# Kernel optimization log

Hardware: AMD Instinct MI355X
Metric: run time of the kernel (lower is better)

The kernel has to match this reference:

```python
import jax, jax.numpy as jnp
import numpy as np

# Base model: 2-layer ReLU MLP, D->H->O, state flattened as [w1, b1, w2, b2]
D, H, O = 32, 64, 1
T = 1024          # xtype_size (number of tickers)
M = 8             # mesa_parameter_size
N = 32768         # rows
S = H * D + H + O * H + O  # 2177, flattened state size


def setup_inputs() -> dict:
    key = jax.random.key(0)
    ks = jax.random.split(key, 6)
    x = jax.random.normal(ks[0], (N, D), dtype=jnp.float32)
    ticker = jax.random.randint(ks[1], (N,), 0, T, dtype=jnp.int32)
    mesa_layer_weight = jax.random.uniform(ks[2], (M, T), jnp.float32, -0.1, 0.1)
    meta_layer_weight = jax.random.uniform(ks[3], (S, M), jnp.float32, -0.1, 0.1)
    meta_layer_bias = jnp.zeros((S,), jnp.float32)
    base_state = jax.random.normal(ks[4], (S,), dtype=jnp.float32) * 0.05
    return {"x": x, "ticker": ticker,
            "mesa_layer_weight": mesa_layer_weight,
            "meta_layer_weight": meta_layer_weight,
            "meta_layer_bias": meta_layer_bias,
            "base_state": base_state}


def _unflatten(states):
    # states: [T, S] -> per-ticker MLP params
    i0 = H * D
    i1 = i0 + H
    i2 = i1 + O * H
    w1 = states[:, :i0].reshape(T, H, D)
    b1 = states[:, i0:i1]                  # [T, H]
    w2 = states[:, i1:i2].reshape(T, O, H)
    b2 = states[:, i2:]                    # [T, O]
    return w1, b1, w2, b2


def reference(x, ticker, mesa_layer_weight, meta_layer_weight, meta_layer_bias, base_state):
    # F.linear(one_hot_i, mesa_W) selects column i -> all mesa states = mesa_W.T : [T, M]
    # temp = meta_W @ mesa_state for every ticker at once: [T, S]
    temps = jnp.einsum('mt,sm->ts', mesa_layer_weight, meta_layer_weight)
    # allow_meta mask is all-ones (allow_meta_structure=None); dropout p=0 is identity
    states = base_state[None, :] + meta_layer_bias[None, :] + temps  # [T, S]
    w1, b1, w2, b2 = _unflatten(states)
    # gather per-row ticker params and run the base MLP forward
    h = jax.nn.relu(jnp.einsum('nd,nhd->nh', x, w1[ticker]) + b1[ticker])  # [N, H]
    out = jnp.einsum('nh,noh->no', h, w2[ticker]) + b2[ticker]             # [N, O]
    return out
```

## Files before the change

kernel.cpp:

```cpp
#include <hip/hip_runtime.h>


#define DD 32
#define TT 1024
#define MM 8
#define KB 8

__global__ __launch_bounds__(1024, 4) void fused_kernel(
    const float* __restrict__ x,
    const int*   __restrict__ ticker,
    const float* __restrict__ mesa,
    const float* __restrict__ metaw,
    const float* __restrict__ metab,
    const float* __restrict__ base,
    float* __restrict__ out)
{
    __shared__ float4 U4[32 * 2 * 64];
    __shared__ float4 B1q[8 * 64];
    __shared__ float4 Ub1[2 * 64];
    __shared__ float4 U2q[2 * 64];
    __shared__ float  B1b[64];
    __shared__ float  B2b[64];

    const int tid  = threadIdx.x;
    const int lane = tid & 63;
    const int dm   = tid >> 6;

    #pragma unroll
    for (int i2 = 0; i2 < 4; ++i2) {
        int idx = dm * 4 + i2;
        int d = idx >> 1, m4 = idx & 1;
        U4[(d * 2 + m4) * 64 + lane] =
            *(const float4*)(metaw + ((lane * 32 + d) * MM + m4 * 4));
    }
    if (dm < 8) {
        int s0 = lane * 32 + dm * 4;
        float4 bv = *(const float4*)(base  + s0);
        float4 mv = *(const float4*)(metab + s0);
        B1q[dm * 64 + lane] = make_float4(bv.x + mv.x, bv.y + mv.y, bv.z + mv.z, bv.w + mv.w);
    } else if (dm < 10) {
        int m4 = dm - 8;
        Ub1[m4 * 64 + lane] = *(const float4*)(metaw + ((2048 + lane) * MM + m4 * 4));
    } else if (dm < 12) {
        int m4 = dm - 10;
        U2q[m4 * 64 + lane] = *(const float4*)(metaw + ((2112 + lane) * MM + m4 * 4));
    } else if (dm == 12) {
        B1b[lane] = base[2048 + lane] + metab[2048 + lane];
    } else if (dm == 13) {
        B2b[lane] = base[2112 + lane] + metab[2112 + lane];
    }
    __syncthreads();

    const int n0 = blockIdx.x * 128 + dm * KB;

    float xr[4];
    #pragma unroll
    for (int r = 0; r < 4; ++r) xr[r] = x[n0 * DD + r * 64 + lane];

    float4 g0[KB], g1[KB];
    float  c0[KB];
    #pragma unroll
    for (int i = 0; i < KB; ++i) {
        g0[i] = make_float4(0.f, 0.f, 0.f, 0.f);
        g1[i] = make_float4(0.f, 0.f, 0.f, 0.f);
        c0[i] = 0.f;
    }

    for (int dq = 0; dq < 8; ++dq) {
        float4 bq = B1q[dq * 64 + lane];
        #pragma unroll
        for (int dd = 0; dd < 4; ++dd) {
            int d = dq * 4 + dd;
            float4 u0 = U4[(d * 2 + 0) * 64 + lane];
            float4 u1 = U4[(d * 2 + 1) * 64 + lane];
            float bs = (dd == 0) ? bq.x : (dd == 1) ? bq.y : (dd == 2) ? bq.z : bq.w;
            #pragma unroll
            for (int i = 0; i < KB; ++i) {
                int lidx = (i & 1) * 32 + d;
                float xv = __uint_as_float(
                    __builtin_amdgcn_readlane(__float_as_uint(xr[i >> 1]), lidx));
                c0[i]   = fmaf(xv, bs,   c0[i]);
                g0[i].x = fmaf(xv, u0.x, g0[i].x);
                g0[i].y = fmaf(xv, u0.y, g0[i].y);
                g0[i].z = fmaf(xv, u0.z, g0[i].z);
                g0[i].w = fmaf(xv, u0.w, g0[i].w);
                g1[i].x = fmaf(xv, u1.x, g1[i].x);
                g1[i].y = fmaf(xv, u1.y, g1[i].y);
                g1[i].z = fmaf(xv, u1.z, g1[i].z);
                g1[i].w = fmaf(xv, u1.w, g1[i].w);
            }
        }
    }

    float4 ub1a = Ub1[0 * 64 + lane], ub1b = Ub1[1 * 64 + lane];
    float4 u2a  = U2q[0 * 64 + lane], u2b  = U2q[1 * 64 + lane];
    float  b1base = B1b[lane], b2base = B2b[lane];
    float4 w2m0 = *(const float4*)(metaw + 2176 * MM);
    float4 w2m1 = *(const float4*)(metaw + 2176 * MM + 4);
    float  b2c  = base[2176] + metab[2176];

    #pragma unroll
    for (int i = 0; i < KB; ++i) {
        int n = n0 + i;
        int t = ticker[n];
        float mi[8];
        #pragma unroll
        for (int m = 0; m < 8; ++m) mi[m] = mesa[m * TT + t];

        float b1 = b1base
                 + mi[0] * ub1a.x + mi[1] * ub1a.y + mi[2] * ub1a.z + mi[3] * ub1a.w
                 + mi[4] * ub1b.x + mi[5] * ub1b.y + mi[6] * ub1b.z + mi[7] * ub1b.w;
        float h = c0[i] + b1
                 + mi[0] * g0[i].x + mi[1] * g0[i].y + mi[2] * g0[i].z + mi[3] * g0[i].w
                 + mi[4] * g1[i].x + mi[5] * g1[i].y + mi[6] * g1[i].z + mi[7] * g1[i].w;
        h = fmaxf(h, 0.f);
        float w2 = b2base
                 + mi[0] * u2a.x + mi[1] * u2a.y + mi[2] * u2a.z + mi[3] * u2a.w
                 + mi[4] * u2b.x + mi[5] * u2b.y + mi[6] * u2b.z + mi[7] * u2b.w;
        float p = h * w2;
        #pragma unroll
        for (int off = 32; off >= 1; off >>= 1)
            p += __shfl_down(p, off, 64);
        if (lane == 0) {
            float b2 = b2c
                 + mi[0] * w2m0.x + mi[1] * w2m0.y + mi[2] * w2m0.z + mi[3] * w2m0.w
                 + mi[4] * w2m1.x + mi[5] * w2m1.y + mi[6] * w2m1.z + mi[7] * w2m1.w;
            out[n] = p + b2;
        }
    }
}

extern "C" void kernel_launch(void* const* d_in, const int* in_sizes, int n_in,
                              void* d_out, int out_size, void* d_ws, size_t ws_size,
                              hipStream_t stream) {
    const float* x      = (const float*)d_in[0];
    const int*   ticker = (const int*)  d_in[1];
    const float* mesa   = (const float*)d_in[2];
    const float* metaw  = (const float*)d_in[3];
    const float* metab  = (const float*)d_in[4];
    const float* base   = (const float*)d_in[5];
    float* out = (float*)d_out;

    fused_kernel<<<256, 1024, 0, stream>>>(x, ticker, mesa, metaw, metab, base, out);
}
```

Before: 87.40 us.

## Materialize per-ticker MLP states and group rows by ticker scan

Adds a state kernel that builds every ticker's full MLP parameters (W1, b1, w2, b2) in workspace and packs tickers as 16-bit values. An apply kernel then gives one ticker to each block pair: it keeps W1 in registers and scans all rows with ballots to find the matching ones. This removes the per-row low-rank reconstruction FMAs of the fused kernel. In exchange it writes about 8MB of state, and every block rescans the whole ticker array, about 2048 blocks times 64KB of reads. Matched rows also load x with scalar per-lane reads. The old fused kernel stays as a fallback when the workspace is too small.

```diff
diff --git a/kernel.cpp b/kernel.cpp
--- a/kernel.cpp
+++ b/kernel.cpp
@@ -5,6 +5,118 @@
 #define TT 1024
 #define MM 8
 #define KB 8
+
+__global__ __launch_bounds__(256, 4) void state_kernel(
+    const float* __restrict__ mesa,
+    const float* __restrict__ metaw,
+    const float* __restrict__ metab,
+    const float* __restrict__ base,
+    const int*   __restrict__ ticker,
+    float* __restrict__ ws)
+{
+    const int t    = blockIdx.x;
+    const int lane = threadIdx.x & 63;
+    const int w    = threadIdx.x >> 6;
+
+    float* W1S = ws;
+    float* B1S = ws + TT * 2048;
+    float* W2S = B1S + TT * 64;
+    float* B2S = W2S + TT * 64;
+    unsigned short* tick16 = (unsigned short*)(B2S + TT);
+
+    float mm[8];
+    #pragma unroll
+    for (int m = 0; m < 8; ++m) mm[m] = mesa[m * TT + t];
+
+    #pragma unroll
+    for (int dd = 0; dd < 8; ++dd) {
+        int d = w * 8 + dd;
+        int s = lane * 32 + d;
+        const float4 u0 = *(const float4*)(metaw + s * MM);
+        const float4 u1 = *(const float4*)(metaw + s * MM + 4);
+        float v = base[s] + metab[s]
+                + mm[0]*u0.x + mm[1]*u0.y + mm[2]*u0.z + mm[3]*u0.w
+                + mm[4]*u1.x + mm[5]*u1.y + mm[6]*u1.z + mm[7]*u1.w;
+        W1S[t * 2048 + d * 64 + lane] = v;
+    }
+
+    if (w == 0) {
+        int s = 2048 + lane;
+        const float4 u0 = *(const float4*)(metaw + s * MM);
+        const float4 u1 = *(const float4*)(metaw + s * MM + 4);
+        B1S[t * 64 + lane] = base[s] + metab[s]
+                + mm[0]*u0.x + mm[1]*u0.y + mm[2]*u0.z + mm[3]*u0.w
+                + mm[4]*u1.x + mm[5]*u1.y + mm[6]*u1.z + mm[7]*u1.w;
+    } else if (w == 1) {
+        int s = 2112 + lane;
+        const float4 u0 = *(const float4*)(metaw + s * MM);
+        const float4 u1 = *(const float4*)(metaw + s * MM + 4);
+        W2S[t * 64 + lane] = base[s] + metab[s]
+                + mm[0]*u0.x + mm[1]*u0.y + mm[2]*u0.z + mm[3]*u0.w
+                + mm[4]*u1.x + mm[5]*u1.y + mm[6]*u1.z + mm[7]*u1.w;
+    } else if (w == 2) {
+        if (lane == 0) {
+            const float4 u0 = *(const float4*)(metaw + 2176 * MM);
+            const float4 u1 = *(const float4*)(metaw + 2176 * MM + 4);
+            B2S[t] = base[2176] + metab[2176]
+                + mm[0]*u0.x + mm[1]*u0.y + mm[2]*u0.z + mm[3]*u0.w
+                + mm[4]*u1.x + mm[5]*u1.y + mm[6]*u1.z + mm[7]*u1.w;
+        }
+    } else {
+        if (lane < 32) tick16[t * 32 + lane] = (unsigned short)ticker[t * 32 + lane];
+    }
+}
+
+__global__ __launch_bounds__(256, 8) void apply_kernel(
+    const float* __restrict__ x,
+    const float* __restrict__ ws,
+    float* __restrict__ out)
+{
+    const int lane = threadIdx.x & 63;
+    const int w    = threadIdx.x >> 6;
+    const int t    = blockIdx.x >> 1;
+    const int half = blockIdx.x & 1;
+
+    const float* W1S = ws;
+    const float* B1S = ws + TT * 2048;
+    const float* W2S = B1S + TT * 64;
+    const float* B2S = W2S + TT * 64;
+    const unsigned short* tick16 = (const unsigned short*)(B2S + TT);
+
+    float w1r[32];
+    #pragma unroll
+    for (int d = 0; d < 32; ++d) w1r[d] = W1S[t * 2048 + d * 64 + lane];
+    const float b1r = B1S[t * 64 + lane];
+    const float w2r = W2S[t * 64 + lane];
+    const float b2v = B2S[t];
+
+    const unsigned short tu = (unsigned short)t;
+    const int base0 = half * 16384 + w * 4096;
+
+    for (int c = 0; c < 4096; c += 64) {
+        int n = base0 + c + lane;
+        unsigned long long m = __ballot(tick16[n] == tu);
+        while (m) {
+            int b = __ffsll(m) - 1;
+            m &= (m - 1);
+            int nn = base0 + c + b;
+            const float* xp = x + (nn << 5);
+            float a0 = 0.f, a1 = 0.f, a2 = 0.f, a3 = 0.f;
+            #pragma unroll
+            for (int d = 0; d < 32; d += 4) {
+                a0 = fmaf(xp[d + 0], w1r[d + 0], a0);
+                a1 = fmaf(xp[d + 1], w1r[d + 1], a1);
+                a2 = fmaf(xp[d + 2], w1r[d + 2], a2);
+                a3 = fmaf(xp[d + 3], w1r[d + 3], a3);
+            }
+            float h = fmaxf((a0 + a1) + (a2 + a3) + b1r, 0.f) * w2r;
+            #pragma unroll
+            for (int off = 32; off >= 1; off >>= 1)
+                h += __shfl_down(h, off, 64);
+            if (lane == 0) out[nn] = h + b2v;
+        }
+    }
+}
 
 __global__ __launch_bounds__(1024, 4) void fused_kernel(
     const float* __restrict__ x,
@@ -141,5 +253,13 @@
     const float* base   = (const float*)d_in[5];
     float* out = (float*)d_out;
 
-    fused_kernel<<<256, 1024, 0, stream>>>(x, ticker, mesa, metaw, metab, base, out);
-}
+    const size_t need = (size_t)(TT * 2048 + TT * 64 + TT * 64 + TT) * sizeof(float)
+                      + (size_t)32768 * sizeof(unsigned short);
+
+    if (ws_size >= need) {
+        state_kernel<<<TT, 256, 0, stream>>>(mesa, metaw, metab, base, ticker, (float*)d_ws);
+        apply_kernel<<<2 * TT, 256, 0, stream>>>(x, (const float*)d_ws, out);
+    } else {
+        fused_kernel<<<256, 1024, 0, stream>>>(x, ticker, mesa, metaw, metab, base, out);
+    }
+}
```

Measured after the change: 110.2 us. 26.1% more time.

## Assign one block per ticker and scan rows with ballot to find its rows

Applied to the files above, without the earlier changes.

The kernel is restructured so each block owns one ticker. It first builds that ticker's full MLP parameter vector in padded shared memory. Each wave then scans a slice of the ticker array, ballots for matching rows, and evaluates the MLP only for those rows. This drops the old per-row algebraic expansion (a 32x8 outer-product accumulation for every row) in favour of direct weight materialization. The cost is that every block re-reads the entire ticker array, and each matched row is handled serially with dependent loads and shuffle reductions.

```diff
diff --git a/kernel.cpp b/kernel.cpp
--- a/kernel.cpp
+++ b/kernel.cpp
@@ -1,12 +1,11 @@
 #include <hip/hip_runtime.h>
 
 
-#define DD 32
 #define TT 1024
-#define MM 8
-#define KB 8
 
-__global__ __launch_bounds__(1024, 4) void fused_kernel(
+__device__ __forceinline__ int pidx(int s) { return s + (s >> 5); }
+
+__global__ __launch_bounds__(512, 8) void fused_owner_kernel(
     const float* __restrict__ x,
     const int*   __restrict__ ticker,
     const float* __restrict__ mesa,
@@ -15,117 +14,72 @@
     const float* __restrict__ base,
     float* __restrict__ out)
 {
-    __shared__ float4 U4[32 * 2 * 64];
-    __shared__ float4 B1q[8 * 64];
-    __shared__ float4 Ub1[2 * 64];
-    __shared__ float4 U2q[2 * 64];
-    __shared__ float  B1b[64];
-    __shared__ float  B2b[64];
+    __shared__ float sm[2304];
 
+    const int t    = blockIdx.x;
     const int tid  = threadIdx.x;
     const int lane = tid & 63;
-    const int dm   = tid >> 6;
+    const int w    = tid >> 6;
+
+    float mm[8];
+    #pragma unroll
+    for (int m = 0; m < 8; ++m) mm[m] = mesa[m * TT + t];
 
     #pragma unroll
-    for (int i2 = 0; i2 < 4; ++i2) {
-        int idx = dm * 4 + i2;
-        int d = idx >> 1, m4 = idx & 1;
-        U4[(d * 2 + m4) * 64 + lane] =
-            *(const float4*)(metaw + ((lane * 32 + d) * MM + m4 * 4));
-    }
-    if (dm < 8) {
-        int s0 = lane * 32 + dm * 4;
-        float4 bv = *(const float4*)(base  + s0);
-        float4 mv = *(const float4*)(metab + s0);
-        B1q[dm * 64 + lane] = make_float4(bv.x + mv.x, bv.y + mv.y, bv.z + mv.z, bv.w + mv.w);
-    } else if (dm < 10) {
-        int m4 = dm - 8;
-        Ub1[m4 * 64 + lane] = *(const float4*)(metaw + ((2048 + lane) * MM + m4 * 4));
-    } else if (dm < 12) {
-        int m4 = dm - 10;
-        U2q[m4 * 64 + lane] = *(const float4*)(metaw + ((2112 + lane) * MM + m4 * 4));
-    } else if (dm == 12) {
-        B1b[lane] = base[2048 + lane] + metab[2048 + lane];
-    } else if (dm == 13) {
-        B2b[lane] = base[2112 + lane] + metab[2112 + lane];
+    for (int k = 0; k < 5; ++k) {
+        int s = tid + k * 512;
+        if (s < 2177) {
+            const float4 u0 = *(const float4*)(metaw + s * 8);
+            const float4 u1 = *(const float4*)(metaw + s * 8 + 4);
+            float v = base[s] + metab[s]
+                    + mm[0]*u0.x + mm[1]*u0.y + mm[2]*u0.z + mm[3]*u0.w
+                    + mm[4]*u1.x + mm[5]*u1.y + mm[6]*u1.z + mm[7]*u1.w;
+            sm[pidx(s)] = v;
+        }
     }
     __syncthreads();
 
-    const int n0 = blockIdx.x * 128 + dm * KB;
+    const int   jb  = lane * 33;
+    const float b1r = sm[pidx(2048 + lane)];
+    const float w2r = sm[pidx(2112 + lane)];
+    const float b2v = sm[pidx(2176)];
 
-    float xr[4];
-    #pragma unroll
-    for (int r = 0; r < 4; ++r) xr[r] = x[n0 * DD + r * 64 + lane];
+    const int   nbase = w * 4096;
+    const int4* tick4 = (const int4*)ticker + (nbase >> 2);
 
-    float4 g0[KB], g1[KB];
-    float  c0[KB];
-    #pragma unroll
-    for (int i = 0; i < KB; ++i) {
-        g0[i] = make_float4(0.f, 0.f, 0.f, 0.f);
-        g1[i] = make_float4(0.f, 0.f, 0.f, 0.f);
-        c0[i] = 0.f;
-    }
+    #pragma unroll 2
+    for (int c = 0; c < 4096; c += 256) {
+        const int4 tv = tick4[(c >> 2) + lane];
+        unsigned long long m0 = __ballot(tv.x == t);
+        unsigned long long m1 = __ballot(tv.y == t);
+        unsigned long long m2 = __ballot(tv.z == t);
+        unsigned long long m3 = __ballot(tv.w == t);
 
-    for (int dq = 0; dq < 8; ++dq) {
-        float4 bq = B1q[dq * 64 + lane];
         #pragma unroll
-        for (int dd = 0; dd < 4; ++dd) {
-            int d = dq * 4 + dd;
-            float4 u0 = U4[(d * 2 + 0) * 64 + lane];
-            float4 u1 = U4[(d * 2 + 1) * 64 + lane];
-            float bs = (dd == 0) ? bq.x : (dd == 1) ? bq.y : (dd == 2) ? bq.z : bq.w;
-            #pragma unroll
-            for (int i = 0; i < KB; ++i) {
-                int lidx = (i & 1) * 32 + d;
-                float xv = __uint_as_float(
-                    __builtin_amdgcn_readlane(__float_as_uint(xr[i >> 1]), lidx));
-                c0[i]   = fmaf(xv, bs,   c0[i]);
-                g0[i].x = fmaf(xv, u0.x, g0[i].x);
-                g0[i].y = fmaf(xv, u0.y, g0[i].y);
-                g0[i].z = fmaf(xv, u0.z, g0[i].z);
-                g0[i].w = fmaf(xv, u0.w, g0[i].w);
-                g1[i].x = fmaf(xv, u1.x, g1[i].x);
-                g1[i].y = fmaf(xv, u1.y, g1[i].y);
-                g1[i].z = fmaf(xv, u1.z, g1[i].z);
-                g1[i].w = fmaf(xv, u1.w, g1[i].w);
+        for (int comp = 0; comp < 4; ++comp) {
+            unsigned long long m = (comp == 0) ? m0 : (comp == 1) ? m1
+                                 : (comp == 2) ? m2 : m3;
+            while (m) {
+                const int b = __ffsll(m) - 1;
+                m &= (m - 1);
+                const int nn = nbase + c + b * 4 + comp;
+                const float* xp = x + (nn << 5);
+
+                float a0 = 0.f, a1 = 0.f, a2 = 0.f, a3 = 0.f;
+                #pragma unroll
+                for (int q = 0; q < 8; ++q) {
+                    const float4 xv = *(const float4*)(xp + q * 4);
+                    a0 = fmaf(xv.x, sm[jb + q * 4 + 0], a0);
+                    a1 = fmaf(xv.y, sm[jb + q * 4 + 1], a1);
+                    a2 = fmaf(xv.z, sm[jb + q * 4 + 2], a2);
+                    a3 = fmaf(xv.w, sm[jb + q * 4 + 3], a3);
+                }
+                float h = fmaxf((a0 + a1) + (a2 + a3) + b1r, 0.f) * w2r;
+                #pragma unroll
+                for (int off = 32; off >= 1; off >>= 1)
+                    h += __shfl_down(h, off, 64);
+                if (lane == 0) out[nn] = h + b2v;
             }
-        }
-    }
-
-    float4 ub1a = Ub1[0 * 64 + lane], ub1b = Ub1[1 * 64 + lane];
-    float4 u2a  = U2q[0 * 64 + lane], u2b  = U2q[1 * 64 + lane];
-    float  b1base = B1b[lane], b2base = B2b[lane];
-    float4 w2m0 = *(const float4*)(metaw + 2176 * MM);
-    float4 w2m1 = *(const float4*)(metaw + 2176 * MM + 4);
-    float  b2c  = base[2176] + metab[2176];
-
-    #pragma unroll
-    for (int i = 0; i < KB; ++i) {
-        int n = n0 + i;
-        int t = ticker[n];
-        float mi[8];
-        #pragma unroll
-        for (int m = 0; m < 8; ++m) mi[m] = mesa[m * TT + t];
-
-        float b1 = b1base
-                 + mi[0] * ub1a.x + mi[1] * ub1a.y + mi[2] * ub1a.z + mi[3] * ub1a.w
-                 + mi[4] * ub1b.x + mi[5] * ub1b.y + mi[6] * ub1b.z + mi[7] * ub1b.w;
-        float h = c0[i] + b1
-                 + mi[0] * g0[i].x + mi[1] * g0[i].y + mi[2] * g0[i].z + mi[3] * g0[i].w
-                 + mi[4] * g1[i].x + mi[5] * g1[i].y + mi[6] * g1[i].z + mi[7] * g1[i].w;
-        h = fmaxf(h, 0.f);
-        float w2 = b2base
-                 + mi[0] * u2a.x + mi[1] * u2a.y + mi[2] * u2a.z + mi[3] * u2a.w
-                 + mi[4] * u2b.x + mi[5] * u2b.y + mi[6] * u2b.z + mi[7] * u2b.w;
-        float p = h * w2;
-        #pragma unroll
-        for (int off = 32; off >= 1; off >>= 1)
-            p += __shfl_down(p, off, 64);
-        if (lane == 0) {
-            float b2 = b2c
-                 + mi[0] * w2m0.x + mi[1] * w2m0.y + mi[2] * w2m0.z + mi[3] * w2m0.w
-                 + mi[4] * w2m1.x + mi[5] * w2m1.y + mi[6] * w2m1.z + mi[7] * w2m1.w;
-            out[n] = p + b2;
         }
     }
 }
@@ -141,5 +95,5 @@
     const float* base   = (const float*)d_in[5];
     float* out = (float*)d_out;
 
-    fused_kernel<<<256, 1024, 0, stream>>>(x, ticker, mesa, metaw, metab, base, out);
+    fused_owner_kernel<<<TT, 512, 0, stream>>>(x, ticker, mesa, metaw, metab, base, out);
 }
```

Result: slower. 91.07 us (+4.2%).
